# Kernel optimization log

Hardware: AMD Instinct MI355X
Metric: run time of the kernel (lower is better)

The kernel has to match this reference:

```python
import jax, jax.numpy as jnp
import numpy as np

IMG_H, IMG_W = 800, 1216   # input image size (stride-32 backbone)
FH, FW = 25, 38            # feature map spatial dims
C = 2048                   # feature channels (100352 = 2048*7*7)
N_BOXES = 2000             # RPN proposals
N_KEEP = 8                 # hard-coded `for i in range(0, 8)` in source
NMS_THRESH = 0.6


def _pairwise_iou(box, boxes):
    # box [4] vs boxes [N,4], corner (x1,y1,x2,y2) format, torchvision convention
    ix1 = jnp.maximum(box[0], boxes[:, 0])
    iy1 = jnp.maximum(box[1], boxes[:, 1])
    ix2 = jnp.minimum(box[2], boxes[:, 2])
    iy2 = jnp.minimum(box[3], boxes[:, 3])
    inter = jnp.clip(ix2 - ix1, 0.0) * jnp.clip(iy2 - iy1, 0.0)
    a1 = (box[2] - box[0]) * (box[3] - box[1])
    a2 = (boxes[:, 2] - boxes[:, 0]) * (boxes[:, 3] - boxes[:, 1])
    return inter / (a1 + a2 - inter)


def _adaptive_maxpool_roi(feat, x, y, w, h):
    # feat [C,FH,FW]; pool window rows [y, y+h), cols [x, x+w) down to 7x7
    # PyTorch AdaptiveMaxPool2d: cell i covers [floor(i*h/7), ceil((i+1)*h/7))
    i = jnp.arange(7)
    r0 = y + (i * h) // 7
    r1 = y + ((i + 1) * h + 6) // 7
    c0 = x + (i * w) // 7
    c1 = x + ((i + 1) * w + 6) // 7
    rows = jnp.arange(feat.shape[1])
    cols = jnp.arange(feat.shape[2])
    rmask = (rows[None, :] >= r0[:, None]) & (rows[None, :] < r1[:, None])  # [7,FH]
    cmask = (cols[None, :] >= c0[:, None]) & (cols[None, :] < c1[:, None])  # [7,FW]
    # row reduce: [C,7,FW], then col reduce: [C,7,7]
    t = jnp.where(rmask[None, :, :, None], feat[:, None, :, :], -jnp.inf).max(axis=2)
    out = jnp.where(cmask[None, None, :, :], t[:, :, None, :], -jnp.inf).max(axis=3)
    return out


def setup_inputs() -> dict:
    key = jax.random.key(0)
    ks = jax.random.split(key, 12)
    feat_map = jax.random.normal(ks[0], (1, C, FH, FW), dtype=jnp.float32)
    # proposals fully inside the image (so index_inside keeps them)
    x1 = jax.random.uniform(ks[1], (N_BOXES,), minval=0.0, maxval=IMG_W - 256.0)
    y1 = jax.random.uniform(ks[2], (N_BOXES,), minval=0.0, maxval=IMG_H - 256.0)
    bw = jax.random.uniform(ks[3], (N_BOXES,), minval=16.0, maxval=256.0)
    bh = jax.random.uniform(ks[4], (N_BOXES,), minval=16.0, maxval=256.0)
    rois = jnp.stack([x1, y1, x1 + bw, y1 + bh], axis=1).astype(jnp.float32)
    scores = jax.random.uniform(ks[5], (N_BOXES, 2), dtype=jnp.float32)
    s = 0.01  # nn.init.normal_(w, 0, 0.01)
    return {
        "feat_map": feat_map,
        "rois": rois,
        "scores": scores,
        "w1": jax.random.normal(ks[6], (4096, 100352), dtype=jnp.float32) * s,
        "b1": jnp.zeros((4096,), jnp.float32),
        "w2": jax.random.normal(ks[7], (4096, 4096), dtype=jnp.float32) * s,
        "b2": jnp.zeros((4096,), jnp.float32),
        "wc": jax.random.normal(ks[8], (81, 4096), dtype=jnp.float32) * s,
        "bc": jnp.zeros((81,), jnp.float32),
        "wl": jax.random.normal(ks[9], (324, 4096), dtype=jnp.float32) * s,
        "bl": jnp.zeros((324,), jnp.float32),
    }


def reference(feat_map, rois, scores, w1, b1, w2, b2, wc, bc, wl, bl):
    feat = feat_map[0]  # [C,FH,FW]
    # index_inside filter
    valid = (rois[:, 0] >= 0) & (rois[:, 1] >= 0) & (rois[:, 2] <= IMG_W) & (rois[:, 3] <= IMG_H)
    fg = scores[:, 1]
    # greedy NMS: first N_KEEP survivors at IoU 0.6 == torchvision.ops.nms(...)[:8]
    alive = valid
    sels = []
    for _ in range(N_KEEP):
        m = jnp.where(alive, fg, -jnp.inf)
        s = jnp.argmax(m)
        sels.append(s)
        iou = _pairwise_iou(rois[s], rois)
        alive = alive & (iou <= NMS_THRESH)
    sels = jnp.stack(sels)
    b = rois[sels] / 32.0  # [8,4]
    # faithful to source: x,y,w,h = int(x+0.5), int(y+0.5), int(w+1), int(h+1)
    x = jnp.floor(b[:, 0] + 0.5).astype(jnp.int32)
    y = jnp.floor(b[:, 1] + 0.5).astype(jnp.int32)
    w = jnp.floor(b[:, 2] + 1.0).astype(jnp.int32)
    h = jnp.floor(b[:, 3] + 1.0).astype(jnp.int32)
    bad = (x < 0) | (x >= FW) | (y < 0) | (y >= FH) | (w < 1) | (x + w > FW) | (h < 1) | (y + h > FH)
    # fallback: pool the entire feature map (roi = feat_map[0])
    x = jnp.where(bad, 0, x)
    y = jnp.where(bad, 0, y)
    w = jnp.where(bad, FW, w)
    h = jnp.where(bad, FH, h)
    pooled = jax.vmap(lambda xx, yy, ww, hh: _adaptive_maxpool_roi(feat, xx, yy, ww, hh))(x, y, w, h)  # [8,C,7,7]
    flat = pooled.reshape(N_KEEP, -1)  # [8,100352]
    o = flat @ w1.T + b1   # no activation in the original
    o = o @ w2.T + b2
    roi_scores = o @ wc.T + bc  # [8,81]
    roi_locs = o @ wl.T + bl    # [8,324]
    return jnp.concatenate([roi_scores, roi_locs], axis=-1)  # [8,405]
```

## Files before the change

### kernel.cpp

```cpp
#include <hip/hip_runtime.h>
#include <cstddef>
#include <math.h>

typedef float v4 __attribute__((ext_vector_type(4)));

#define IMG_H 800
#define IMG_W 1216
#define FH 25
#define FWW 38
#define NBOX 2000
#define NKEEP 8
#define D1 100352
#define K1 4096
#define NSLICE 16
#define DPS (D1/NSLICE)

__device__ inline v4 ldnt4(const float* p) {
    return __builtin_nontemporal_load((const v4*)p);
}

__global__ __launch_bounds__(256) void nms_sel_kernel(const float* __restrict__ rois,
                                                      const float* __restrict__ scores,
                                                      int* __restrict__ roi_out) {
    __shared__ float4 s_box[NBOX];
    __shared__ float  s_fg[NBOX];
    __shared__ float  red_v[256];
    __shared__ int    red_i[256];
    __shared__ int    s_sels[NKEEP];
    const int tid = threadIdx.x;

    for (int i = tid; i < NBOX; i += 256) {
        float x1 = rois[i*4+0], y1 = rois[i*4+1], x2 = rois[i*4+2], y2 = rois[i*4+3];
        s_box[i] = make_float4(x1, y1, x2, y2);
        bool valid = (x1 >= 0.f) && (y1 >= 0.f) && (x2 <= (float)IMG_W) && (y2 <= (float)IMG_H);
        s_fg[i] = valid ? scores[i*2+1] : -INFINITY;
    }
    __syncthreads();

    for (int it = 0; it < NKEEP; ++it) {
        float bv = -INFINITY; int bi = NBOX;
        for (int i = tid; i < NBOX; i += 256) {
            float v = s_fg[i];
            if (v > bv || (v == bv && i < bi)) { bv = v; bi = i; }
        }
        red_v[tid] = bv; red_i[tid] = bi;
        __syncthreads();
        for (int off = 128; off > 0; off >>= 1) {
            if (tid < off) {
                float v = red_v[tid+off]; int ii = red_i[tid+off];
                if (v > red_v[tid] || (v == red_v[tid] && ii < red_i[tid])) {
                    red_v[tid] = v; red_i[tid] = ii;
                }
            }
            __syncthreads();
        }
        int s = red_i[0];
        if (s >= NBOX) s = 0;
        if (tid == 0) s_sels[it] = s;

        float4 bs = s_box[s];
        float a1 = (bs.z - bs.x) * (bs.w - bs.y);
        for (int i = tid; i < NBOX; i += 256) {
            float4 b = s_box[i];
            float ix1 = fmaxf(bs.x, b.x), iy1 = fmaxf(bs.y, b.y);
            float ix2 = fminf(bs.z, b.z), iy2 = fminf(bs.w, b.w);
            float inter = fmaxf(ix2 - ix1, 0.f) * fmaxf(iy2 - iy1, 0.f);
            float a2 = (b.z - b.x) * (b.w - b.y);
            float iou = inter / (a1 + a2 - inter);
            if (!(iou <= 0.6f)) s_fg[i] = -INFINITY;
        }
        __syncthreads();
    }

    if (tid < NKEEP) {
        int s = s_sels[tid];
        float4 b = s_box[s];
        int x = (int)floorf(b.x / 32.0f + 0.5f);
        int y = (int)floorf(b.y / 32.0f + 0.5f);
        int w = (int)floorf(b.z / 32.0f + 1.0f);
        int h = (int)floorf(b.w / 32.0f + 1.0f);
        bool bad = (x < 0) || (x >= FWW) || (y < 0) || (y >= FH) ||
                   (w < 1) || (x + w > FWW) || (h < 1) || (y + h > FH);
        if (bad) { x = 0; y = 0; w = FWW; h = FH; }
        roi_out[tid*4+0] = x; roi_out[tid*4+1] = y;
        roi_out[tid*4+2] = w; roi_out[tid*4+3] = h;
    }
}

__global__ __launch_bounds__(256) void roi_pool_kernel(const float* __restrict__ feat,
                                                       const int* __restrict__ roi_out,
                                                       float* __restrict__ pooled) {
    int idx = blockIdx.x * 256 + threadIdx.x;
    if (idx >= NKEEP * D1) return;
    int r    = idx / D1;
    int rem  = idx - r * D1;
    int c    = rem / 49;
    int cell = rem - c * 49;
    int i = cell / 7;
    int j = cell - i * 7;
    int x = roi_out[r*4+0], y = roi_out[r*4+1], w = roi_out[r*4+2], h = roi_out[r*4+3];
    int r0 = y + (i * h) / 7;
    int r1 = y + ((i + 1) * h + 6) / 7;
    int c0 = x + (j * w) / 7;
    int c1 = x + ((j + 1) * w + 6) / 7;
    const float* fc = feat + (size_t)c * (FH * FWW);
    float m = -INFINITY;
    for (int rr = r0; rr < r1; ++rr) {
        const float* fr = fc + rr * FWW;
        for (int cc2 = c0; cc2 < c1; ++cc2) m = fmaxf(m, fr[cc2]);
    }
    pooled[idx] = m;
}

__global__ __launch_bounds__(256) void init_bias8_kernel(const float* __restrict__ b,
                                                         float* __restrict__ o, int K) {
    int i = blockIdx.x * 256 + threadIdx.x;
    if (i < NKEEP * K) o[i] = b[i & (K - 1)];
}

__global__ __launch_bounds__(256) void fc1_kernel(const float* __restrict__ w1,
                                                  const float* __restrict__ flat,
                                                  float* __restrict__ o1) {
    const int kb = blockIdx.x >> 4;
    const int ds = blockIdx.x & 15;
    const int tid = threadIdx.x;
    const int kq = tid >> 4;
    const int dl = tid & 15;
    const int k0 = kb * 64 + kq * 4;
    const int dbase = ds * DPS + dl * 4;

    const float* wp = w1 + (size_t)k0 * D1 + dbase;
    const float* fp = flat + dbase;

    float acc[4][8];
    #pragma unroll
    for (int a = 0; a < 4; ++a)
        #pragma unroll
        for (int n = 0; n < 8; ++n) acc[a][n] = 0.f;

    v4 wa[4];
    #pragma unroll
    for (int a = 0; a < 4; ++a) wa[a] = ldnt4(wp + (size_t)a * D1);

    for (int itn = 0; itn < DPS / 64; ++itn) {
        const int off  = itn * 64;
        const int offn = (itn < DPS / 64 - 1) ? off + 64 : off;

        v4 fv[8];
        #pragma unroll
        for (int n = 0; n < 8; ++n) fv[n] = *(const v4*)(fp + (size_t)n * D1 + off);

        v4 wb[4];
        #pragma unroll
        for (int a = 0; a < 4; ++a) wb[a] = ldnt4(wp + (size_t)a * D1 + offn);

        #pragma unroll
        for (int n = 0; n < 8; ++n) {
            acc[0][n] += wa[0][0]*fv[n][0] + wa[0][1]*fv[n][1] + wa[0][2]*fv[n][2] + wa[0][3]*fv[n][3];
            acc[1][n] += wa[1][0]*fv[n][0] + wa[1][1]*fv[n][1] + wa[1][2]*fv[n][2] + wa[1][3]*fv[n][3];
            acc[2][n] += wa[2][0]*fv[n][0] + wa[2][1]*fv[n][1] + wa[2][2]*fv[n][2] + wa[2][3]*fv[n][3];
            acc[3][n] += wa[3][0]*fv[n][0] + wa[3][1]*fv[n][1] + wa[3][2]*fv[n][2] + wa[3][3]*fv[n][3];
        }

        #pragma unroll
        for (int a = 0; a < 4; ++a) wa[a] = wb[a];
    }

    #pragma unroll
    for (int a = 0; a < 4; ++a) {
        #pragma unroll
        for (int n = 0; n < 8; ++n) {
            float v = acc[a][n];
            v += __shfl_xor(v, 1);
            v += __shfl_xor(v, 2);
            v += __shfl_xor(v, 4);
            v += __shfl_xor(v, 8);
            if (dl == 0) atomicAdd(&o1[n * K1 + k0 + a], v);
        }
    }
}

__global__ __launch_bounds__(256) void fc2_kernel(const float* __restrict__ w2,
                                                  const float* __restrict__ o1,
                                                  const float* __restrict__ b2,
                                                  float* __restrict__ o2) {
    int gw   = (blockIdx.x * 256 + threadIdx.x) >> 6;
    int lane = threadIdx.x & 63;
    if (gw >= K1) return;
    const float* wr = w2 + (size_t)gw * K1;
    const v4* fo = (const v4*)o1;
    float acc[8];
    #pragma unroll
    for (int n = 0; n < 8; ++n) acc[n] = 0.f;
    for (int itn = 0; itn < K1 / 256; ++itn) {
        v4 wv = ldnt4(wr + (itn * 64 + lane) * 4);
        #pragma unroll
        for (int n = 0; n < 8; ++n) {
            v4 f = fo[n * (K1/4) + itn * 64 + lane];
            acc[n] += wv[0]*f[0] + wv[1]*f[1] + wv[2]*f[2] + wv[3]*f[3];
        }
    }
    #pragma unroll
    for (int n = 0; n < 8; ++n) {
        float v = acc[n];
        #pragma unroll
        for (int m = 32; m >= 1; m >>= 1) v += __shfl_xor(v, m);
        if (lane == 0) o2[n * K1 + gw] = v + b2[gw];
    }
}

__global__ __launch_bounds__(256) void fc3_kernel(const float* __restrict__ wc,
                                                  const float* __restrict__ bc,
                                                  const float* __restrict__ wl,
                                                  const float* __restrict__ bl,
                                                  const float* __restrict__ o2,
                                                  float* __restrict__ out) {
    int gw   = (blockIdx.x * 256 + threadIdx.x) >> 6;
    int lane = threadIdx.x & 63;
    if (gw >= 405) return;
    const float* wrow; float bias;
    if (gw < 81) { wrow = wc + (size_t)gw * K1;        bias = bc[gw]; }
    else         { wrow = wl + (size_t)(gw - 81) * K1; bias = bl[gw - 81]; }
    const v4* fo = (const v4*)o2;
    float acc[8];
    #pragma unroll
    for (int n = 0; n < 8; ++n) acc[n] = 0.f;
    for (int itn = 0; itn < K1 / 256; ++itn) {
        v4 wv = ldnt4(wrow + (itn * 64 + lane) * 4);
        #pragma unroll
        for (int n = 0; n < 8; ++n) {
            v4 f = fo[n * (K1/4) + itn * 64 + lane];
            acc[n] += wv[0]*f[0] + wv[1]*f[1] + wv[2]*f[2] + wv[3]*f[3];
        }
    }
    #pragma unroll
    for (int n = 0; n < 8; ++n) {
        float v = acc[n];
        #pragma unroll
        for (int m = 32; m >= 1; m >>= 1) v += __shfl_xor(v, m);
        if (lane == 0) out[n * 405 + gw] = v + bias;
    }
}

extern "C" void kernel_launch(void* const* d_in, const int* in_sizes, int n_in,
                              void* d_out, int out_size, void* d_ws, size_t ws_size,
                              hipStream_t stream) {
    const float* feat   = (const float*)d_in[0];
    const float* rois   = (const float*)d_in[1];
    const float* scores = (const float*)d_in[2];
    const float* w1     = (const float*)d_in[3];
    const float* b1     = (const float*)d_in[4];
    const float* w2     = (const float*)d_in[5];
    const float* b2     = (const float*)d_in[6];
    const float* wc     = (const float*)d_in[7];
    const float* bc     = (const float*)d_in[8];
    const float* wl     = (const float*)d_in[9];
    const float* bl     = (const float*)d_in[10];
    float* out = (float*)d_out;

    int*   roi_out = (int*)d_ws;
    float* pooled  = (float*)d_ws + 256;
    float* o1      = pooled + (size_t)NKEEP * D1;
    float* o2      = o1 + NKEEP * K1;

    nms_sel_kernel<<<1, 256, 0, stream>>>(rois, scores, roi_out);
    roi_pool_kernel<<<(NKEEP * D1 + 255) / 256, 256, 0, stream>>>(feat, roi_out, pooled);
    init_bias8_kernel<<<(NKEEP * K1 + 255) / 256, 256, 0, stream>>>(b1, o1, K1);
    fc1_kernel<<<64 * NSLICE, 256, 0, stream>>>(w1, pooled, o1);
    fc2_kernel<<<K1 / 4, 256, 0, stream>>>(w2, o1, b2, o2);
    fc3_kernel<<<(405 * 64 + 255) / 256, 256, 0, stream>>>(wc, bc, wl, bl, o2, out);
}
```

Baseline: 385.9 us.

## Stage fc1 activations in LDS, deepen weight prefetch, increase D slices

```diff
diff --git a/kernel.cpp b/kernel.cpp
--- a/kernel.cpp
+++ b/kernel.cpp
@@ -12,8 +12,8 @@
 #define NKEEP 8
 #define D1 100352
 #define K1 4096
-#define NSLICE 16
-#define DPS (D1/NSLICE)
+#define NSLICE 56
+#define DPS 1792
 
 __device__ inline v4 ldnt4(const float* p) {
     return __builtin_nontemporal_load((const v4*)p);
@@ -121,16 +121,25 @@
 __global__ __launch_bounds__(256) void fc1_kernel(const float* __restrict__ w1,
                                                   const float* __restrict__ flat,
                                                   float* __restrict__ o1) {
-    const int kb = blockIdx.x >> 4;
-    const int ds = blockIdx.x & 15;
+    __shared__ float s_f[NKEEP][DPS];
+
+    const int bid = blockIdx.x;
+    const int kb  = bid / NSLICE;
+    const int ds  = bid - kb * NSLICE;
     const int tid = threadIdx.x;
-    const int kq = tid >> 4;
-    const int dl = tid & 15;
-    const int k0 = kb * 64 + kq * 4;
-    const int dbase = ds * DPS + dl * 4;
-
-    const float* wp = w1 + (size_t)k0 * D1 + dbase;
-    const float* fp = flat + dbase;
+    const int kq  = tid >> 4;
+    const int dl  = tid & 15;
+    const int k0  = kb * 64 + kq * 4;
+    const int dbase = ds * DPS;
+
+    for (int i = tid; i < (NKEEP * DPS) / 4; i += 256) {
+        int n  = i / (DPS / 4);
+        int c4 = i - n * (DPS / 4);
+        *(v4*)&s_f[n][c4 * 4] = *(const v4*)(flat + (size_t)n * D1 + dbase + c4 * 4);
+    }
+    __syncthreads();
+
+    const float* wp = w1 + (size_t)k0 * D1 + dbase + dl * 4;
 
     float acc[4][8];
     #pragma unroll
@@ -138,21 +147,23 @@
         #pragma unroll
         for (int n = 0; n < 8; ++n) acc[a][n] = 0.f;
 
-    v4 wa[4];
+    v4 wa[4], wb[4];
     #pragma unroll
     for (int a = 0; a < 4; ++a) wa[a] = ldnt4(wp + (size_t)a * D1);
+    #pragma unroll
+    for (int a = 0; a < 4; ++a) wb[a] = ldnt4(wp + (size_t)a * D1 + 64);
 
     for (int itn = 0; itn < DPS / 64; ++itn) {
         const int off  = itn * 64;
-        const int offn = (itn < DPS / 64 - 1) ? off + 64 : off;
+        const int offp = (itn < DPS / 64 - 2) ? off + 128 : 0;
 
         v4 fv[8];
         #pragma unroll
-        for (int n = 0; n < 8; ++n) fv[n] = *(const v4*)(fp + (size_t)n * D1 + off);
-
-        v4 wb[4];
-        #pragma unroll
-        for (int a = 0; a < 4; ++a) wb[a] = ldnt4(wp + (size_t)a * D1 + offn);
+        for (int n = 0; n < 8; ++n) fv[n] = *(const v4*)&s_f[n][dl * 4 + off];
+
+        v4 wc_[4];
+        #pragma unroll
+        for (int a = 0; a < 4; ++a) wc_[a] = ldnt4(wp + (size_t)a * D1 + offp);
 
         #pragma unroll
         for (int n = 0; n < 8; ++n) {
@@ -163,7 +174,7 @@
         }
 
         #pragma unroll
-        for (int a = 0; a < 4; ++a) wa[a] = wb[a];
+        for (int a = 0; a < 4; ++a) { wa[a] = wb[a]; wb[a] = wc_[a]; }
     }
 
     #pragma unroll
```

Result: slower. 422.2 us (+9.4%).
